# Optimization experiments

Hardware: AMD Instinct MI355X
Metric: run time of the kernel (lower is better)

Reference implementation:

```python
import jax, jax.numpy as jnp
import numpy as np

LN_EPS = 1e-5


def setup_inputs() -> dict:
    key = jax.random.key(0)
    ks = jax.random.split(key, 8)
    N, c_z, H, C = 256, 128, 4, 32
    s = 0.02  # small init scale for stable softmax
    return {
        "z": jax.random.normal(ks[0], (N, N, c_z), dtype=jnp.float32),
        "ln_g": jnp.ones((c_z,), jnp.float32),
        "ln_b": jnp.zeros((c_z,), jnp.float32),
        "Wb": jax.random.normal(ks[1], (c_z, H), dtype=jnp.float32) * s,
        "Wq": jax.random.normal(ks[2], (c_z, H, C), dtype=jnp.float32) * s,
        "Wk": jax.random.normal(ks[3], (c_z, H, C), dtype=jnp.float32) * s,
        "Wv": jax.random.normal(ks[4], (c_z, H, C), dtype=jnp.float32) * s,
        "Wg": jax.random.normal(ks[5], (c_z, H, C), dtype=jnp.float32) * s,
        "bg": jnp.ones((H, C), jnp.float32),
        "Wo": jax.random.normal(ks[6], (H, C, c_z), dtype=jnp.float32) * s,
        "bo": jnp.zeros((c_z,), jnp.float32),
    }


def reference(z, ln_g, ln_b, Wb, Wq, Wk, Wv, Wg, bg, Wo, bo):
    # TriangleAttention, node_type='starting_node' (Algorithm 13).
    # z: (N, N, c_z)
    C = Wq.shape[-1]
    # LayerNorm over c_z
    mu = jnp.mean(z, axis=-1, keepdims=True)
    var = jnp.var(z, axis=-1, keepdims=True)
    x = (z - mu) * jax.lax.rsqrt(var + LN_EPS) * ln_g + ln_b
    # pairwise additive bias: b[h, j, k] = (x @ Wb)[j, k, h]
    b = jnp.einsum('jkz,zh->hjk', x, Wb)
    # per-head projections; attention over second residue axis (-2),
    # first residue axis i acts as batch
    q = jnp.einsum('ijz,zhc->ijhc', x, Wq)
    k = jnp.einsum('ijz,zhc->ijhc', x, Wk)
    v = jnp.einsum('ijz,zhc->ijhc', x, Wv)
    scores = jnp.einsum('iqhc,ikhc->hiqk', q, k) / jnp.sqrt(jnp.asarray(C, x.dtype))
    scores = scores + b[:, None, :, :]  # broadcast bias over batch axis i
    a = jax.nn.softmax(scores, axis=-1)  # (h, i, q, k)
    o = jnp.einsum('hiqk,ikhc->iqhc', a, v)
    g = jax.nn.sigmoid(jnp.einsum('ijz,zhc->ijhc', x, Wg) + bg)
    o = o * g
    out = jnp.einsum('iqhc,hcz->iqz', o, Wo) + bo
    return out
```

## Files before the change

### kernel.cpp

```cpp
#include <hip/hip_runtime.h>
#include <hip/hip_bf16.h>
#include <math.h>


#define NN 256
#define CZ 128

typedef __attribute__((ext_vector_type(8))) short bf16x8;
typedef __attribute__((ext_vector_type(4))) float f32x4;

__device__ __forceinline__ f32x4 mfma16(bf16x8 a, bf16x8 b, f32x4 c) {
  return __builtin_amdgcn_mfma_f32_16x16x32_bf16(a, b, c, 0, 0, 0);
}
__device__ __forceinline__ unsigned short f2bf(float f) {
  unsigned b = __float_as_uint(f);
  return (unsigned short)((b + 0x7FFFu + ((b >> 16) & 1u)) >> 16);
}
__device__ __forceinline__ float bf2f(unsigned short u) { return __uint_as_float((unsigned)u << 16); }
__device__ __forceinline__ unsigned packbf(float a, float b) {
  return (unsigned)f2bf(a) | ((unsigned)f2bf(b) << 16);
}
__device__ __forceinline__ bf16x8 remap_frag(unsigned pk00, unsigned pk01,
                                             unsigned pk10, unsigned pk11,
                                             int srcA, int srcB, bool hi) {
  unsigned a0 = (unsigned)__shfl((int)pk00, srcA);
  unsigned b0 = (unsigned)__shfl((int)pk10, srcA);
  unsigned a1 = (unsigned)__shfl((int)pk01, srcA);
  unsigned b1 = (unsigned)__shfl((int)pk11, srcA);
  unsigned a2 = (unsigned)__shfl((int)pk00, srcB);
  unsigned b2 = (unsigned)__shfl((int)pk10, srcB);
  unsigned a3 = (unsigned)__shfl((int)pk01, srcB);
  unsigned b3 = (unsigned)__shfl((int)pk11, srcB);
  uint4 u;
  u.x = hi ? b0 : a0;
  u.y = hi ? b1 : a1;
  u.z = hi ? b2 : a2;
  u.w = hi ? b3 : a3;
  return *(bf16x8*)&u;
}

__global__ __launch_bounds__(128) void k_prep(const float* __restrict__ Wq, const float* __restrict__ Wk,
                                              const float* __restrict__ Wv, const float* __restrict__ Wg,
                                              const float* __restrict__ Wo, unsigned short* __restrict__ Wt) {
  int sec = blockIdx.y, n = blockIdx.x, t = threadIdx.x;
  const float* s = sec == 0 ? Wq : sec == 1 ? Wk : sec == 2 ? Wv : sec == 3 ? Wg : Wo;
  Wt[(sec * 128 + n) * 128 + t] = f2bf(s[t * 128 + n]);
}

__global__ __launch_bounds__(256) void k_ln(const float* __restrict__ z,
                                            const float* __restrict__ ln_g,
                                            const float* __restrict__ ln_b,
                                            const float* __restrict__ Wb,
                                            unsigned short* __restrict__ xb,
                                            float* __restrict__ bN) {
  int wave = threadIdx.x >> 6, lane = threadIdx.x & 63;
  int pos = blockIdx.x * 4 + wave;
  float2 v = ((const float2*)(z + (size_t)pos * CZ))[lane];
  float s = v.x + v.y, sq = v.x * v.x + v.y * v.y;
#pragma unroll
  for (int o = 1; o < 64; o <<= 1) { s += __shfl_xor(s, o); sq += __shfl_xor(sq, o); }
  float mean = s * (1.0f / CZ);
  float var = sq * (1.0f / CZ) - mean * mean;
  float rstd = rsqrtf(var + 1e-5f);
  int c0 = lane * 2;
  float x0 = (v.x - mean) * rstd * ln_g[c0] + ln_b[c0];
  float x1 = (v.y - mean) * rstd * ln_g[c0 + 1] + ln_b[c0 + 1];
  unsigned pk = (unsigned)f2bf(x0) | ((unsigned)f2bf(x1) << 16);
  ((unsigned*)(xb + (size_t)pos * CZ))[lane] = pk;
  float4 w0 = *(const float4*)(Wb + c0 * 4);
  float4 w1 = *(const float4*)(Wb + (c0 + 1) * 4);
  float b0 = x0 * w0.x + x1 * w1.x;
  float b1 = x0 * w0.y + x1 * w1.y;
  float b2 = x0 * w0.z + x1 * w1.z;
  float b3 = x0 * w0.w + x1 * w1.w;
#pragma unroll
  for (int o = 1; o < 64; o <<= 1) {
    b0 += __shfl_xor(b0, o); b1 += __shfl_xor(b1, o);
    b2 += __shfl_xor(b2, o); b3 += __shfl_xor(b3, o);
  }
  if (lane == 0) {
    const float L2E = 1.4426950408889634f;
    int j = pos >> 8, kk = pos & 255;
    bN[0 * 65536 + j * 256 + kk] = b0 * L2E;
    bN[1 * 65536 + j * 256 + kk] = b1 * L2E;
    bN[2 * 65536 + j * 256 + kk] = b2 * L2E;
    bN[3 * 65536 + j * 256 + kk] = b3 * L2E;
  }
}

__global__ __launch_bounds__(256, 4) void k_head(const unsigned short* __restrict__ xb,
                                                 const unsigned short* __restrict__ Wt,
                                                 const float* __restrict__ bN,
                                                 const float* __restrict__ bg,
                                                 unsigned short* __restrict__ og) {
  __shared__ unsigned short ks[256][40];
  __shared__ unsigned short vt[32][264];
  int i = blockIdx.x, h = blockIdx.y;
  int t = threadIdx.x, w = t >> 6, lane = t & 63, l16 = lane & 15, g = lane >> 4;
  const int srcA = l16 + 32 * (g & 1);
  const int srcB = srcA + 16;
  const bool hi = g >= 2;
  const float sc2 = 0.25503486f;

  bf16x8 qa[4];
  unsigned gtp[4][2][2];

#pragma unroll
  for (int rh = 0; rh < 2; rh++) {
    int r0 = w * 64 + rh * 32;
    bf16x8 xa[2][4];
#pragma unroll
    for (int m = 0; m < 2; m++)
#pragma unroll
      for (int kt = 0; kt < 4; kt++)
        xa[m][kt] = *(const bf16x8*)(xb + (size_t)(i * 256 + r0 + m * 16 + l16) * CZ + kt * 32 + g * 8);

    {
      bf16x8 wf[2][4];
#pragma unroll
      for (int n = 0; n < 2; n++)
#pragma unroll
        for (int kt = 0; kt < 4; kt++)
          wf[n][kt] = *(const bf16x8*)(Wt + (size_t)(128 + h * 32 + n * 16 + l16) * CZ + kt * 32 + g * 8);
      f32x4 d[2][2];
#pragma unroll
      for (int m = 0; m < 2; m++)
#pragma unroll
        for (int n = 0; n < 2; n++) d[m][n] = (f32x4){0.f, 0.f, 0.f, 0.f};
#pragma unroll
      for (int kt = 0; kt < 4; kt++)
#pragma unroll
        for (int m = 0; m < 2; m++)
#pragma unroll
          for (int n = 0; n < 2; n++) d[m][n] = mfma16(wf[n][kt], xa[m][kt], d[m][n]);
#pragma unroll
      for (int m = 0; m < 2; m++)
#pragma unroll
        for (int n = 0; n < 2; n++) {
          ushort4 pk4;
          pk4.x = f2bf(d[m][n][0]); pk4.y = f2bf(d[m][n][1]);
          pk4.z = f2bf(d[m][n][2]); pk4.w = f2bf(d[m][n][3]);
          *(ushort4*)&ks[r0 + m * 16 + l16][n * 16 + g * 4] = pk4;
        }
    }
    {
      bf16x8 wf[2][4];
#pragma unroll
      for (int n = 0; n < 2; n++)
#pragma unroll
        for (int kt = 0; kt < 4; kt++)
          wf[n][kt] = *(const bf16x8*)(Wt + (size_t)(256 + h * 32 + n * 16 + l16) * CZ + kt * 32 + g * 8);
      f32x4 d[2][2];
#pragma unroll
      for (int m = 0; m < 2; m++)
#pragma unroll
        for (int n = 0; n < 2; n++) d[m][n] = (f32x4){0.f, 0.f, 0.f, 0.f};
#pragma unroll
      for (int kt = 0; kt < 4; kt++)
#pragma unroll
        for (int m = 0; m < 2; m++)
#pragma unroll
          for (int n = 0; n < 2; n++) d[m][n] = mfma16(xa[m][kt], wf[n][kt], d[m][n]);
#pragma unroll
      for (int m = 0; m < 2; m++)
#pragma unroll
        for (int n = 0; n < 2; n++) {
          ushort4 pk4;
          pk4.x = f2bf(d[m][n][0]); pk4.y = f2bf(d[m][n][1]);
          pk4.z = f2bf(d[m][n][2]); pk4.w = f2bf(d[m][n][3]);
          *(ushort4*)&vt[n * 16 + l16][r0 + m * 16 + g * 4] = pk4;
        }
    }
    {
      bf16x8 wf[2][4];
#pragma unroll
      for (int n = 0; n < 2; n++)
#pragma unroll
        for (int kt = 0; kt < 4; kt++)
          wf[n][kt] = *(const bf16x8*)(Wt + (size_t)(0 + h * 32 + n * 16 + l16) * CZ + kt * 32 + g * 8);
      f32x4 d[2][2];
#pragma unroll
      for (int m = 0; m < 2; m++)
#pragma unroll
        for (int n = 0; n < 2; n++) d[m][n] = (f32x4){0.f, 0.f, 0.f, 0.f};
#pragma unroll
      for (int kt = 0; kt < 4; kt++)
#pragma unroll
        for (int m = 0; m < 2; m++)
#pragma unroll
          for (int n = 0; n < 2; n++) d[m][n] = mfma16(wf[n][kt], xa[m][kt], d[m][n]);
#pragma unroll
      for (int m = 0; m < 2; m++) {
        unsigned pk00 = packbf(d[m][0][0] * sc2, d[m][0][1] * sc2);
        unsigned pk01 = packbf(d[m][0][2] * sc2, d[m][0][3] * sc2);
        unsigned pk10 = packbf(d[m][1][0] * sc2, d[m][1][1] * sc2);
        unsigned pk11 = packbf(d[m][1][2] * sc2, d[m][1][3] * sc2);
        qa[rh * 2 + m] = remap_frag(pk00, pk01, pk10, pk11, srcA, srcB, hi);
      }
    }
    {
      bf16x8 wf[2][4];
#pragma unroll
      for (int n = 0; n < 2; n++)
#pragma unroll
        for (int kt = 0; kt < 4; kt++)
          wf[n][kt] = *(const bf16x8*)(Wt + (size_t)(384 + h * 32 + n * 16 + l16) * CZ + kt * 32 + g * 8);
      f32x4 d[2][2];
#pragma unroll
      for (int m = 0; m < 2; m++)
#pragma unroll
        for (int n = 0; n < 2; n++) d[m][n] = (f32x4){0.f, 0.f, 0.f, 0.f};
#pragma unroll
      for (int kt = 0; kt < 4; kt++)
#pragma unroll
        for (int m = 0; m < 2; m++)
#pragma unroll
          for (int n = 0; n < 2; n++) d[m][n] = mfma16(wf[n][kt], xa[m][kt], d[m][n]);
#pragma unroll
      for (int n = 0; n < 2; n++) {
        float4 bgv = *(const float4*)(bg + h * 32 + n * 16 + g * 4);
#pragma unroll
        for (int m = 0; m < 2; m++) {
          float s0 = 1.0f / (1.0f + __expf(-(d[m][n][0] + bgv.x)));
          float s1 = 1.0f / (1.0f + __expf(-(d[m][n][1] + bgv.y)));
          float s2 = 1.0f / (1.0f + __expf(-(d[m][n][2] + bgv.z)));
          float s3 = 1.0f / (1.0f + __expf(-(d[m][n][3] + bgv.w)));
          gtp[rh * 2 + m][n][0] = packbf(s0, s1);
          gtp[rh * 2 + m][n][1] = packbf(s2, s3);
        }
      }
    }
  }
  __syncthreads();

  f32x4 oacc[4][2];
  float lsum[4];
#pragma unroll
  for (int qB = 0; qB < 4; qB++) {
    lsum[qB] = 0.f;
    oacc[qB][0] = (f32x4){0.f, 0.f, 0.f, 0.f};
    oacc[qB][1] = (f32x4){0.f, 0.f, 0.f, 0.f};
  }
  const float* bb = bN + (size_t)h * 65536;
#pragma unroll 2
  for (int kc = 0; kc < 8; kc++) {
    bf16x8 kb[2], vb[2];
#pragma unroll
    for (int n = 0; n < 2; n++) kb[n] = *(const bf16x8*)&ks[kc * 32 + n * 16 + l16][g * 8];
#pragma unroll
    for (int n = 0; n < 2; n++) vb[n] = *(const bf16x8*)&vt[n * 16 + l16][kc * 32 + g * 8];
#pragma unroll
    for (int qB = 0; qB < 4; qB++) {
      int qrow = w * 64 + qB * 16 + l16;
      float4 c0 = *(const float4*)(bb + (size_t)qrow * 256 + kc * 32 + 0 * 16 + g * 4);
      float4 c1 = *(const float4*)(bb + (size_t)qrow * 256 + kc * 32 + 1 * 16 + g * 4);
      f32x4 s0 = mfma16(kb[0], qa[qB], (f32x4){c0.x, c0.y, c0.z, c0.w});
      f32x4 s1 = mfma16(kb[1], qa[qB], (f32x4){c1.x, c1.y, c1.z, c1.w});
      float p0 = exp2f(s0[0]), p1 = exp2f(s0[1]), p2 = exp2f(s0[2]), p3 = exp2f(s0[3]);
      float p4 = exp2f(s1[0]), p5 = exp2f(s1[1]), p6 = exp2f(s1[2]), p7 = exp2f(s1[3]);
      lsum[qB] += ((p0 + p1) + (p2 + p3)) + ((p4 + p5) + (p6 + p7));
      unsigned pk00 = packbf(p0, p1), pk01 = packbf(p2, p3);
      unsigned pk10 = packbf(p4, p5), pk11 = packbf(p6, p7);
      bf16x8 pf = remap_frag(pk00, pk01, pk10, pk11, srcA, srcB, hi);
      oacc[qB][0] = mfma16(vb[0], pf, oacc[qB][0]);
      oacc[qB][1] = mfma16(vb[1], pf, oacc[qB][1]);
    }
  }
#pragma unroll
  for (int qB = 0; qB < 4; qB++) {
    float l = lsum[qB];
    l += __shfl_xor(l, 16);
    l += __shfl_xor(l, 32);
    float inv = 1.0f / l;
#pragma unroll
    for (int nc = 0; nc < 2; nc++) {
      float g0 = bf2f((unsigned short)(gtp[qB][nc][0] & 0xffffu));
      float g1 = bf2f((unsigned short)(gtp[qB][nc][0] >> 16));
      float g2 = bf2f((unsigned short)(gtp[qB][nc][1] & 0xffffu));
      float g3 = bf2f((unsigned short)(gtp[qB][nc][1] >> 16));
      ushort4 pk4;
      pk4.x = f2bf(oacc[qB][nc][0] * inv * g0);
      pk4.y = f2bf(oacc[qB][nc][1] * inv * g1);
      pk4.z = f2bf(oacc[qB][nc][2] * inv * g2);
      pk4.w = f2bf(oacc[qB][nc][3] * inv * g3);
      *(ushort4*)(og + (size_t)(i * 256 + w * 64 + qB * 16 + l16) * 128 + h * 32 + nc * 16 + g * 4) = pk4;
    }
  }
}

__global__ __launch_bounds__(256) void k_out(const unsigned short* __restrict__ og,
                                             const unsigned short* __restrict__ WoT,
                                             const float* __restrict__ bo,
                                             float* __restrict__ out) {
  int t = threadIdx.x, w = t >> 6, lane = t & 63, l16 = lane & 15, g = lane >> 4;
  int wr = w >> 1, wc = w & 1;
  int pbase = blockIdx.x * 128 + wr * 64;
  int cbase = wc * 64;
  f32x4 acc[4][4];
#pragma unroll
  for (int m = 0; m < 4; m++)
#pragma unroll
    for (int n = 0; n < 4; n++) acc[m][n] = (f32x4){0.f, 0.f, 0.f, 0.f};
#pragma unroll
  for (int kt = 0; kt < 4; kt++) {
    bf16x8 a[4], b[4];
#pragma unroll
    for (int m = 0; m < 4; m++)
      a[m] = *(const bf16x8*)(og + (size_t)(pbase + m * 16 + l16) * 128 + kt * 32 + g * 8);
#pragma unroll
    for (int n = 0; n < 4; n++)
      b[n] = *(const bf16x8*)(WoT + (size_t)(cbase + n * 16 + l16) * 128 + kt * 32 + g * 8);
#pragma unroll
    for (int m = 0; m < 4; m++)
#pragma unroll
      for (int n = 0; n < 4; n++) acc[m][n] = mfma16(a[m], b[n], acc[m][n]);
  }
#pragma unroll
  for (int n = 0; n < 4; n++) {
    int zc = cbase + n * 16 + l16;
    float bv = bo[zc];
#pragma unroll
    for (int m = 0; m < 4; m++) {
#pragma unroll
      for (int r = 0; r < 4; r++)
        out[(size_t)(pbase + m * 16 + g * 4 + r) * 128 + zc] = acc[m][n][r] + bv;
    }
  }
}

extern "C" void kernel_launch(void* const* d_in, const int* in_sizes, int n_in,
                              void* d_out, int out_size, void* d_ws, size_t ws_size,
                              hipStream_t stream) {
  const float* z    = (const float*)d_in[0];
  const float* ln_g = (const float*)d_in[1];
  const float* ln_b = (const float*)d_in[2];
  const float* Wb   = (const float*)d_in[3];
  const float* Wq   = (const float*)d_in[4];
  const float* Wk   = (const float*)d_in[5];
  const float* Wv   = (const float*)d_in[6];
  const float* Wg   = (const float*)d_in[7];
  const float* bg   = (const float*)d_in[8];
  const float* Wo   = (const float*)d_in[9];
  const float* bo   = (const float*)d_in[10];
  float* out = (float*)d_out;

  char* ws = (char*)d_ws;
  unsigned short* xb = (unsigned short*)(ws + 0);
  float*          bN = (float*)(ws + 16777216);
  unsigned short* Wt = (unsigned short*)(ws + 17825792);
  unsigned short* og = (unsigned short*)(ws + 17989632);

  k_prep<<<dim3(128, 5), 128, 0, stream>>>(Wq, Wk, Wv, Wg, Wo, Wt);
  k_ln<<<16384, 256, 0, stream>>>(z, ln_g, ln_b, Wb, xb, bN);
  k_head<<<dim3(256, 4), 256, 0, stream>>>(xb, Wt, bN, bg, og);
  k_out<<<512, 256, 0, stream>>>(og, Wt + 512 * 128, bo, out);
}
```

Before: 213.9 us.

## Restructure LayerNorm, prefetch K/V fragments, stage outputs through LDS

The LayerNorm kernel now assigns four lanes per position with 128-bit loads and stores, replacing the full-wave shuffle reductions, and the grid shrinks to match. k_head loads all x fragments once and loops the row halves inside each projection. It also double-buffers the K/V LDS fragments across key chunks and writes the gated output through LDS so the global stores are coalesced. k_out stages its A tile in LDS before the MFMA loop. Launch bounds move from 4 to 3 waves per SIMD for k_head, trading occupancy for the extra registers.

After: 206.5 us. -3.4%, faster.

```diff
diff --git a/kernel.cpp b/kernel.cpp
--- a/kernel.cpp
+++ b/kernel.cpp
@@ -53,34 +53,56 @@
                                             const float* __restrict__ Wb,
                                             unsigned short* __restrict__ xb,
                                             float* __restrict__ bN) {
-  int wave = threadIdx.x >> 6, lane = threadIdx.x & 63;
-  int pos = blockIdx.x * 4 + wave;
-  float2 v = ((const float2*)(z + (size_t)pos * CZ))[lane];
-  float s = v.x + v.y, sq = v.x * v.x + v.y * v.y;
-#pragma unroll
-  for (int o = 1; o < 64; o <<= 1) { s += __shfl_xor(s, o); sq += __shfl_xor(sq, o); }
+  int t = threadIdx.x, wave = t >> 6, lane = t & 63;
+  int p = blockIdx.x * 64 + wave * 16 + (lane >> 2);
+  int q4 = lane & 3;
+  const float* src = z + (size_t)p * CZ + q4 * 32;
+  float x[32];
+  float s = 0.f, sq = 0.f;
+#pragma unroll
+  for (int e = 0; e < 8; e++) {
+    float4 v = *(const float4*)(src + e * 4);
+    x[e * 4 + 0] = v.x; x[e * 4 + 1] = v.y; x[e * 4 + 2] = v.z; x[e * 4 + 3] = v.w;
+    s += (v.x + v.y) + (v.z + v.w);
+    sq += (v.x * v.x + v.y * v.y) + (v.z * v.z + v.w * v.w);
+  }
+  s += __shfl_xor(s, 1); sq += __shfl_xor(sq, 1);
+  s += __shfl_xor(s, 2); sq += __shfl_xor(sq, 2);
   float mean = s * (1.0f / CZ);
   float var = sq * (1.0f / CZ) - mean * mean;
   float rstd = rsqrtf(var + 1e-5f);
-  int c0 = lane * 2;
-  float x0 = (v.x - mean) * rstd * ln_g[c0] + ln_b[c0];
-  float x1 = (v.y - mean) * rstd * ln_g[c0 + 1] + ln_b[c0 + 1];
-  unsigned pk = (unsigned)f2bf(x0) | ((unsigned)f2bf(x1) << 16);
-  ((unsigned*)(xb + (size_t)pos * CZ))[lane] = pk;
-  float4 w0 = *(const float4*)(Wb + c0 * 4);
-  float4 w1 = *(const float4*)(Wb + (c0 + 1) * 4);
-  float b0 = x0 * w0.x + x1 * w1.x;
-  float b1 = x0 * w0.y + x1 * w1.y;
-  float b2 = x0 * w0.z + x1 * w1.z;
-  float b3 = x0 * w0.w + x1 * w1.w;
-#pragma unroll
-  for (int o = 1; o < 64; o <<= 1) {
-    b0 += __shfl_xor(b0, o); b1 += __shfl_xor(b1, o);
-    b2 += __shfl_xor(b2, o); b3 += __shfl_xor(b3, o);
-  }
-  if (lane == 0) {
+  float b0 = 0.f, b1 = 0.f, b2 = 0.f, b3 = 0.f;
+  unsigned pk[16];
+#pragma unroll
+  for (int e = 0; e < 8; e++) {
+    float4 gv = *(const float4*)(ln_g + q4 * 32 + e * 4);
+    float4 bv = *(const float4*)(ln_b + q4 * 32 + e * 4);
+    float x0 = (x[e * 4 + 0] - mean) * rstd * gv.x + bv.x;
+    float x1 = (x[e * 4 + 1] - mean) * rstd * gv.y + bv.y;
+    float x2 = (x[e * 4 + 2] - mean) * rstd * gv.z + bv.z;
+    float x3 = (x[e * 4 + 3] - mean) * rstd * gv.w + bv.w;
+    pk[e * 2 + 0] = packbf(x0, x1);
+    pk[e * 2 + 1] = packbf(x2, x3);
+    int zr = (q4 * 32 + e * 4) * 4;
+    float4 w0 = *(const float4*)(Wb + zr);
+    float4 w1 = *(const float4*)(Wb + zr + 4);
+    float4 w2 = *(const float4*)(Wb + zr + 8);
+    float4 w3 = *(const float4*)(Wb + zr + 12);
+    b0 += x0 * w0.x + x1 * w1.x + x2 * w2.x + x3 * w3.x;
+    b1 += x0 * w0.y + x1 * w1.y + x2 * w2.y + x3 * w3.y;
+    b2 += x0 * w0.z + x1 * w1.z + x2 * w2.z + x3 * w3.z;
+    b3 += x0 * w0.w + x1 * w1.w + x2 * w2.w + x3 * w3.w;
+  }
+  unsigned* dst = (unsigned*)(xb + (size_t)p * CZ + q4 * 32);
+#pragma unroll
+  for (int u = 0; u < 4; u++) ((uint4*)dst)[u] = ((uint4*)pk)[u];
+  b0 += __shfl_xor(b0, 1); b1 += __shfl_xor(b1, 1);
+  b2 += __shfl_xor(b2, 1); b3 += __shfl_xor(b3, 1);
+  b0 += __shfl_xor(b0, 2); b1 += __shfl_xor(b1, 2);
+  b2 += __shfl_xor(b2, 2); b3 += __shfl_xor(b3, 2);
+  if (q4 == 0) {
     const float L2E = 1.4426950408889634f;
-    int j = pos >> 8, kk = pos & 255;
+    int j = p >> 8, kk = p & 255;
     bN[0 * 65536 + j * 256 + kk] = b0 * L2E;
     bN[1 * 65536 + j * 256 + kk] = b1 * L2E;
     bN[2 * 65536 + j * 256 + kk] = b2 * L2E;
@@ -88,7 +110,7 @@
   }
 }
 
-__global__ __launch_bounds__(256, 4) void k_head(const unsigned short* __restrict__ xb,
+__global__ __launch_bounds__(256, 3) void k_head(const unsigned short* __restrict__ xb,
                                                  const unsigned short* __restrict__ Wt,
                                                  const float* __restrict__ bN,
                                                  const float* __restrict__ bg,
@@ -105,23 +127,22 @@
   bf16x8 qa[4];
   unsigned gtp[4][2][2];
 
-#pragma unroll
-  for (int rh = 0; rh < 2; rh++) {
-    int r0 = w * 64 + rh * 32;
-    bf16x8 xa[2][4];
-#pragma unroll
-    for (int m = 0; m < 2; m++)
-#pragma unroll
-      for (int kt = 0; kt < 4; kt++)
-        xa[m][kt] = *(const bf16x8*)(xb + (size_t)(i * 256 + r0 + m * 16 + l16) * CZ + kt * 32 + g * 8);
-
-    {
-      bf16x8 wf[2][4];
-#pragma unroll
-      for (int n = 0; n < 2; n++)
-#pragma unroll
-        for (int kt = 0; kt < 4; kt++)
-          wf[n][kt] = *(const bf16x8*)(Wt + (size_t)(128 + h * 32 + n * 16 + l16) * CZ + kt * 32 + g * 8);
+  bf16x8 xa[4][4];
+#pragma unroll
+  for (int mm = 0; mm < 4; mm++)
+#pragma unroll
+    for (int kt = 0; kt < 4; kt++)
+      xa[mm][kt] = *(const bf16x8*)(xb + (size_t)(i * 256 + w * 64 + mm * 16 + l16) * CZ + kt * 32 + g * 8);
+
+  {
+    bf16x8 wf[2][4];
+#pragma unroll
+    for (int n = 0; n < 2; n++)
+#pragma unroll
+      for (int kt = 0; kt < 4; kt++)
+        wf[n][kt] = *(const bf16x8*)(Wt + (size_t)(128 + h * 32 + n * 16 + l16) * CZ + kt * 32 + g * 8);
+#pragma unroll
+    for (int rh = 0; rh < 2; rh++) {
       f32x4 d[2][2];
 #pragma unroll
       for (int m = 0; m < 2; m++)
@@ -132,7 +153,7 @@
 #pragma unroll
         for (int m = 0; m < 2; m++)
 #pragma unroll
-          for (int n = 0; n < 2; n++) d[m][n] = mfma16(wf[n][kt], xa[m][kt], d[m][n]);
+          for (int n = 0; n < 2; n++) d[m][n] = mfma16(wf[n][kt], xa[rh * 2 + m][kt], d[m][n]);
 #pragma unroll
       for (int m = 0; m < 2; m++)
 #pragma unroll
@@ -140,16 +161,19 @@
           ushort4 pk4;
           pk4.x = f2bf(d[m][n][0]); pk4.y = f2bf(d[m][n][1]);
           pk4.z = f2bf(d[m][n][2]); pk4.w = f2bf(d[m][n][3]);
-          *(ushort4*)&ks[r0 + m * 16 + l16][n * 16 + g * 4] = pk4;
+          *(ushort4*)&ks[w * 64 + rh * 32 + m * 16 + l16][n * 16 + g * 4] = pk4;
         }
     }
-    {
-      bf16x8 wf[2][4];
-#pragma unroll
-      for (int n = 0; n < 2; n++)
-#pragma unroll
-        for (int kt = 0; kt < 4; kt++)
-          wf[n][kt] = *(const bf16x8*)(Wt + (size_t)(256 + h * 32 + n * 16 + l16) * CZ + kt * 32 + g * 8);
+  }
+  {
+    bf16x8 wf[2][4];
+#pragma unroll
+    for (int n = 0; n < 2; n++)
+#pragma unroll
+      for (int kt = 0; kt < 4; kt++)
+        wf[n][kt] = *(const bf16x8*)(Wt + (size_t)(256 + h * 32 + n * 16 + l16) * CZ + kt * 32 + g * 8);
+#pragma unroll
+    for (int rh = 0; rh < 2; rh++) {
       f32x4 d[2][2];
 #pragma unroll
       for (int m = 0; m < 2; m++)
@@ -160,7 +184,7 @@
 #pragma unroll
         for (int m = 0; m < 2; m++)
 #pragma unroll
-          for (int n = 0; n < 2; n++) d[m][n] = mfma16(xa[m][kt], wf[n][kt], d[m][n]);
+          for (int n = 0; n < 2; n++) d[m][n] = mfma16(xa[rh * 2 + m][kt], wf[n][kt], d[m][n]);
 #pragma unroll
       for (int m = 0; m < 2; m++)
 #pragma unroll
@@ -168,16 +192,19 @@
           ushort4 pk4;
           pk4.x = f2bf(d[m][n][0]); pk4.y = f2bf(d[m][n][1]);
           pk4.z = f2bf(d[m][n][2]); pk4.w = f2bf(d[m][n][3]);
-          *(ushort4*)&vt[n * 16 + l16][r0 + m * 16 + g * 4] = pk4;
+          *(ushort4*)&vt[n * 16 + l16][w * 64 + rh * 32 + m * 16 + g * 4] = pk4;
         }
     }
-    {
-      bf16x8 wf[2][4];
-#pragma unroll
-      for (int n = 0; n < 2; n++)
-#pragma unroll
-        for (int kt = 0; kt < 4; kt++)
-          wf[n][kt] = *(const bf16x8*)(Wt + (size_t)(0 + h * 32 + n * 16 + l16) * CZ + kt * 32 + g * 8);
+  }
+  {
+    bf16x8 wf[2][4];
+#pragma unroll
+    for (int n = 0; n < 2; n++)
+#pragma unroll
+      for (int kt = 0; kt < 4; kt++)
+        wf[n][kt] = *(const bf16x8*)(Wt + (size_t)(0 + h * 32 + n * 16 + l16) * CZ + kt * 32 + g * 8);
+#pragma unroll
+    for (int rh = 0; rh < 2; rh++) {
       f32x4 d[2][2];
 #pragma unroll
       for (int m = 0; m < 2; m++)
@@ -188,7 +215,7 @@
 #pragma unroll
         for (int m = 0; m < 2; m++)
 #pragma unroll
-          for (int n = 0; n < 2; n++) d[m][n] = mfma16(wf[n][kt], xa[m][kt], d[m][n]);
+          for (int n = 0; n < 2; n++) d[m][n] = mfma16(wf[n][kt], xa[rh * 2 + m][kt], d[m][n]);
 #pragma unroll
       for (int m = 0; m < 2; m++) {
         unsigned pk00 = packbf(d[m][0][0] * sc2, d[m][0][1] * sc2);
@@ -198,13 +225,16 @@
         qa[rh * 2 + m] = remap_frag(pk00, pk01, pk10, pk11, srcA, srcB, hi);
       }
     }
-    {
-      bf16x8 wf[2][4];
-#pragma unroll
-      for (int n = 0; n < 2; n++)
-#pragma unroll
-        for (int kt = 0; kt < 4; kt++)
-          wf[n][kt] = *(const bf16x8*)(Wt + (size_t)(384 + h * 32 + n * 16 + l16) * CZ + kt * 32 + g * 8);
+  }
+  {
+    bf16x8 wf[2][4];
+#pragma unroll
+    for (int n = 0; n < 2; n++)
+#pragma unroll
+      for (int kt = 0; kt < 4; kt++)
+        wf[n][kt] = *(const bf16x8*)(Wt + (size_t)(384 + h * 32 + n * 16 + l16) * CZ + kt * 32 + g * 8);
+#pragma unroll
+    for (int rh = 0; rh < 2; rh++) {
       f32x4 d[2][2];
 #pragma unroll
       for (int m = 0; m < 2; m++)
@@ -215,7 +245,7 @@
 #pragma unroll
         for (int m = 0; m < 2; m++)
 #pragma unroll
-          for (int n = 0; n < 2; n++) d[m][n] = mfma16(wf[n][kt], xa[m][kt], d[m][n]);
+          for (int n = 0; n < 2; n++) d[m][n] = mfma16(wf[n][kt], xa[rh * 2 + m][kt], d[m][n]);
 #pragma unroll
       for (int n = 0; n < 2; n++) {
         float4 bgv = *(const float4*)(bg + h * 32 + n * 16 + g * 4);
@@ -242,13 +272,21 @@
     oacc[qB][1] = (f32x4){0.f, 0.f, 0.f, 0.f};
   }
   const float* bb = bN + (size_t)h * 65536;
+  bf16x8 kb[2], vb[2], kbn[2], vbn[2];
+#pragma unroll
+  for (int n = 0; n < 2; n++) {
+    kb[n] = *(const bf16x8*)&ks[0 * 32 + n * 16 + l16][g * 8];
+    vb[n] = *(const bf16x8*)&vt[n * 16 + l16][0 * 32 + g * 8];
+  }
 #pragma unroll 2
   for (int kc = 0; kc < 8; kc++) {
-    bf16x8 kb[2], vb[2];
-#pragma unroll
-    for (int n = 0; n < 2; n++) kb[n] = *(const bf16x8*)&ks[kc * 32 + n * 16 + l16][g * 8];
-#pragma unroll
-    for (int n = 0; n < 2; n++) vb[n] = *(const bf16x8*)&vt[n * 16 + l16][kc * 32 + g * 8];
+    if (kc < 7) {
+#pragma unroll
+      for (int n = 0; n < 2; n++) {
+        kbn[n] = *(const bf16x8*)&ks[(kc + 1) * 32 + n * 16 + l16][g * 8];
+        vbn[n] = *(const bf16x8*)&vt[n * 16 + l16][(kc + 1) * 32 + g * 8];
+      }
+    }
 #pragma unroll
     for (int qB = 0; qB < 4; qB++) {
       int qrow = w * 64 + qB * 16 + l16;
@@ -265,7 +303,10 @@
       oacc[qB][0] = mfma16(vb[0], pf, oacc[qB][0]);
       oacc[qB][1] = mfma16(vb[1], pf, oacc[qB][1]);
     }
-  }
+    kb[0] = kbn[0]; kb[1] = kbn[1]; vb[0] = vbn[0]; vb[1] = vbn[1];
+  }
+  __syncthreads();
+  unsigned short* myst = &ks[w * 64][0];
 #pragma unroll
   for (int qB = 0; qB < 4; qB++) {
     float l = lsum[qB];
@@ -283,19 +324,34 @@
       pk4.y = f2bf(oacc[qB][nc][1] * inv * g1);
       pk4.z = f2bf(oacc[qB][nc][2] * inv * g2);
       pk4.w = f2bf(oacc[qB][nc][3] * inv * g3);
-      *(ushort4*)(og + (size_t)(i * 256 + w * 64 + qB * 16 + l16) * 128 + h * 32 + nc * 16 + g * 4) = pk4;
-    }
-  }
-}
-
-__global__ __launch_bounds__(256) void k_out(const unsigned short* __restrict__ og,
-                                             const unsigned short* __restrict__ WoT,
-                                             const float* __restrict__ bo,
-                                             float* __restrict__ out) {
+      *(ushort4*)&myst[(qB * 16 + l16) * 40 + nc * 16 + g * 4] = pk4;
+    }
+  }
+#pragma unroll
+  for (int e = 0; e < 8; e++) {
+    int row = e * 8 + (lane >> 3), chunk = lane & 7;
+    *(ushort4*)(og + (size_t)(i * 256 + w * 64 + row) * 128 + h * 32 + chunk * 4) =
+        *(const ushort4*)&myst[row * 40 + chunk * 4];
+  }
+}
+
+__global__ __launch_bounds__(256, 4) void k_out(const unsigned short* __restrict__ og,
+                                                const unsigned short* __restrict__ WoT,
+                                                const float* __restrict__ bo,
+                                                float* __restrict__ out) {
+  __shared__ unsigned short ot[128][136];
   int t = threadIdx.x, w = t >> 6, lane = t & 63, l16 = lane & 15, g = lane >> 4;
   int wr = w >> 1, wc = w & 1;
-  int pbase = blockIdx.x * 128 + wr * 64;
-  int cbase = wc * 64;
+  int pbase = blockIdx.x * 128;
+#pragma unroll
+  for (int e = 0; e < 8; e++) {
+    int idx = e * 256 + t;
+    int row = idx >> 4, chunk = idx & 15;
+    uint4 v = *(const uint4*)(og + (size_t)(pbase + row) * 128 + chunk * 8);
+    *(uint4*)&ot[row][chunk * 8] = v;
+  }
+  __syncthreads();
+  int prow = wr * 64, cbase = wc * 64;
   f32x4 acc[4][4];
 #pragma unroll
   for (int m = 0; m < 4; m++)
@@ -306,7 +362,7 @@
     bf16x8 a[4], b[4];
 #pragma unroll
     for (int m = 0; m < 4; m++)
-      a[m] = *(const bf16x8*)(og + (size_t)(pbase + m * 16 + l16) * 128 + kt * 32 + g * 8);
+      a[m] = *(const bf16x8*)&ot[prow + m * 16 + l16][kt * 32 + g * 8];
 #pragma unroll
     for (int n = 0; n < 4; n++)
       b[n] = *(const bf16x8*)(WoT + (size_t)(cbase + n * 16 + l16) * 128 + kt * 32 + g * 8);
@@ -323,7 +379,7 @@
     for (int m = 0; m < 4; m++) {
 #pragma unroll
       for (int r = 0; r < 4; r++)
-        out[(size_t)(pbase + m * 16 + g * 4 + r) * 128 + zc] = acc[m][n][r] + bv;
+        out[(size_t)(pbase + prow + m * 16 + g * 4 + r) * 128 + zc] = acc[m][n][r] + bv;
     }
   }
 }
@@ -351,7 +407,7 @@
   unsigned short* og = (unsigned short*)(ws + 17989632);
 
   k_prep<<<dim3(128, 5), 128, 0, stream>>>(Wq, Wk, Wv, Wg, Wo, Wt);
-  k_ln<<<16384, 256, 0, stream>>>(z, ln_g, ln_b, Wb, xb, bN);
+  k_ln<<<1024, 256, 0, stream>>>(z, ln_g, ln_b, Wb, xb, bN);
   k_head<<<dim3(256, 4), 256, 0, stream>>>(xb, Wt, bN, bg, og);
   k_out<<<512, 256, 0, stream>>>(og, Wt + 512 * 128, bo, out);
 }
```
